# Optimization experiments

Measured on AMD Instinct MI355X. Metric: run time of the kernel, lower is better.

The kernel has to match this reference:

```python
import jax, jax.numpy as jnp
import numpy as np

B, S, D = 4, 2048, 1024


def setup_inputs() -> dict:
    key = jax.random.key(0)
    k1, k2, k3, k4, k5 = jax.random.split(key, 5)
    x = jax.random.normal(k1, (B, S, D), dtype=jnp.float32)
    mask = jax.random.randint(k2, (B, S), 0, 2).astype(jnp.bool_)
    # glorot-uniform-like init as keras add_weight default
    lim = float(np.sqrt(6.0 / (D + D)))
    q_w = jax.random.uniform(k3, (D, D), minval=-lim, maxval=lim, dtype=jnp.float32)
    k_w = jax.random.uniform(k4, (D, D), minval=-lim, maxval=lim, dtype=jnp.float32)
    v_w = jax.random.uniform(k5, (D, D), minval=-lim, maxval=lim, dtype=jnp.float32)
    return {"x": x, "mask": mask, "q_w": q_w, "k_w": k_w, "v_w": v_w}


def reference(x, mask, q_w, k_w, v_w):
    scale = 1.0 / jnp.sqrt(jnp.asarray(x.shape[-1], dtype=x.dtype))
    q = jnp.einsum('bsi,ij->bsj', x, q_w)
    k = jnp.einsum('bsi,ij->bsj', x, k_w)
    y = jnp.einsum('bsi,bzi->bsz', q, k) * scale  # [B,S,S] scores
    # additive mask applied along the query axis, exactly as the source
    m = (~mask).astype(x.dtype)[:, :, None]
    y = y + m * (-1e9)
    v = jnp.einsum('bsi,ij->bsj', x, v_w)
    p = jax.nn.softmax(y, axis=-1)
    return jnp.einsum('bsz,bzi->bsi', p, v)
```

## Files before the change

### kernel.cpp

```cpp
#include <hip/hip_runtime.h>
#include <hip/hip_bf16.h>

typedef __attribute__((ext_vector_type(8))) short short8;
typedef __attribute__((ext_vector_type(4))) float floatx4;

struct ushort4v { unsigned short x, y, z, w; };

static __device__ __forceinline__ unsigned short f2bf(float f) {
    __hip_bfloat16 h = __float2bfloat16(f);
    return *reinterpret_cast<unsigned short*>(&h);
}

static __device__ __forceinline__ float bf2f(unsigned short u) {
    unsigned int v = ((unsigned int)u) << 16;
    return *reinterpret_cast<float*>(&v);
}

#define ASYNC_COPY16(gsrc, ldst)                                                            \
    __builtin_amdgcn_global_load_lds((const __attribute__((address_space(1))) void*)(gsrc), \
                                     (__attribute__((address_space(3))) void*)(ldst), 16, 0, 0)

static __device__ __forceinline__ void block_barrier() {
    asm volatile("" ::: "memory");
    __builtin_amdgcn_s_barrier();
    asm volatile("" ::: "memory");
}

__global__ void mask_detect(const unsigned char* __restrict__ m, int* __restrict__ flag) {
    __shared__ int s_or;
    if (threadIdx.x == 0) s_or = 0;
    __syncthreads();
    int acc = 0;
    for (int i = threadIdx.x; i < 8192; i += 256)
        if (i & 3) acc |= m[i];
    atomicOr(&s_or, acc);
    __syncthreads();
    if (threadIdx.x == 0) *flag = (s_or != 0) ? 1 : 0;
}

__global__ void mask_expand(const void* __restrict__ m, const int* __restrict__ flag,
                            float* __restrict__ keep, int n) {
    int i = blockIdx.x * 256 + threadIdx.x;
    if (i >= n) return;
    bool on;
    if (*flag)
        on = ((const unsigned char*)m)[i] != 0;
    else
        on = ((const int*)m)[i] != 0;
    keep[i] = on ? 1.0f : 0.0f;
}

__global__ __launch_bounds__(256) void convert_f32_bf16(const float* __restrict__ in,
                                                        unsigned short* __restrict__ out, long n4) {
    long i = (long)blockIdx.x * 256 + threadIdx.x;
    if (i >= n4) return;
    float4 v = ((const float4*)in)[i];
    ushort4v o;
    o.x = f2bf(v.x); o.y = f2bf(v.y); o.z = f2bf(v.z); o.w = f2bf(v.w);
    ((ushort4v*)out)[i] = o;
}

__global__ void transpose_w_kernel(const float* __restrict__ w0, const float* __restrict__ w1,
                                   const float* __restrict__ w2, unsigned short* __restrict__ out) {
    __shared__ float t[32][33];
    const float* w = blockIdx.z == 0 ? w0 : (blockIdx.z == 1 ? w1 : w2);
    unsigned short* o = out + (long)blockIdx.z * 1024 * 1024;
    int c0 = blockIdx.x * 32, r0 = blockIdx.y * 32;
    for (int i = threadIdx.y; i < 32; i += 8)
        t[i][threadIdx.x] = w[(long)(r0 + i) * 1024 + c0 + threadIdx.x];
    __syncthreads();
    for (int i = threadIdx.y; i < 32; i += 8)
        o[(long)(c0 + i) * 1024 + r0 + threadIdx.x] = f2bf(t[threadIdx.x][i]);
}

__global__ void transpose_bf16(const unsigned short* __restrict__ in, unsigned short* __restrict__ out,
                               int rows, int cols, long sIn, long sOut) {
    __shared__ unsigned short t[32][34];
    const unsigned short* ib = in + (long)blockIdx.z * sIn;
    unsigned short* ob = out + (long)blockIdx.z * sOut;
    int c0 = blockIdx.x * 32, r0 = blockIdx.y * 32;
    for (int i = threadIdx.y; i < 32; i += 8)
        t[i][threadIdx.x] = ib[(long)(r0 + i) * cols + c0 + threadIdx.x];
    __syncthreads();
    for (int i = threadIdx.y; i < 32; i += 8)
        ob[(long)(c0 + i) * rows + r0 + threadIdx.x] = t[threadIdx.x][i];
}

template <int EPI, int BM>
static __device__ __forceinline__ void gemm8_body(const unsigned short* __restrict__ A,
                                                  const unsigned short* __restrict__ B,
                                                  void* __restrict__ Cv,
                                                  const float* __restrict__ aux,
                                                  int K, int lda, int ldb, int ldc,
                                                  long sA, long sB, long sC, long sAux,
                                                  float scale) {
    constexpr int M_REP = BM / 32;
    constexpr int LA    = BM * 128 / 8192;
    constexpr int LB    = 4;
    constexpr int TILE  = (BM + 256) * 128;
    __shared__ char sm[2 * TILE];

    const int tid = threadIdx.x;
    const int wid = tid >> 6, lane = tid & 63;
    const int wm  = wid >> 2, wn = wid & 3;
    const int fr  = lane & 15, fk = lane >> 4;
    const long m0 = (long)blockIdx.x * BM;
    const long n0 = (long)blockIdx.y * 256;
    const unsigned short* Ab = A + (long)blockIdx.z * sA + m0 * lda;
    const unsigned short* Bb = B + (long)blockIdx.z * sB + n0 * ldb;
    const int NT = K >> 6;

    floatx4 acc[M_REP][4] = {};

    auto stage = [&](int kt) {
        char* dA = sm + (kt & 1) * TILE;
        char* dB = dA + BM * 128;
        const int kb = kt << 6;
#pragma unroll
        for (int i = 0; i < LA; i++) {
            int lam = i * 8192 + tid * 16;
            int lg  = lam ^ (((lam >> 7) & 7) << 4);
            ASYNC_COPY16(Ab + (long)(lg >> 7) * lda + kb + ((lg & 127) >> 1), dA + lam);
        }
#pragma unroll
        for (int i = 0; i < LB; i++) {
            int lam = i * 8192 + tid * 16;
            int lg  = lam ^ (((lam >> 7) & 7) << 4);
            ASYNC_COPY16(Bb + (long)(lg >> 7) * ldb + kb + ((lg & 127) >> 1), dB + lam);
        }
    };

    stage(0);
    stage(1);

    for (int t = 0; t < NT; t++) {
        if (t + 1 < NT) {
            if constexpr (BM == 256) asm volatile("s_waitcnt vmcnt(8)" ::: "memory");
            else                     asm volatile("s_waitcnt vmcnt(6)" ::: "memory");
        } else {
            asm volatile("s_waitcnt vmcnt(0)" ::: "memory");
        }
        block_barrier();

        const char* bA = sm + (t & 1) * TILE;
        const char* bB = bA + BM * 128;
#pragma unroll
        for (int ks = 0; ks < 2; ks++) {
            short8 af[M_REP], bf[4];
#pragma unroll
            for (int mi = 0; mi < M_REP; mi++) {
                int row = wm * (BM / 2) + mi * 16 + fr;
                int c   = (ks * 64 + fk * 16) ^ ((row & 7) << 4);
                af[mi] = *(const short8*)(bA + row * 128 + c);
            }
#pragma unroll
            for (int ni = 0; ni < 4; ni++) {
                int row = wn * 64 + ni * 16 + fr;
                int c   = (ks * 64 + fk * 16) ^ ((row & 7) << 4);
                bf[ni] = *(const short8*)(bB + row * 128 + c);
            }
            __builtin_amdgcn_s_setprio(1);
#pragma unroll
            for (int mi = 0; mi < M_REP; mi++)
#pragma unroll
                for (int ni = 0; ni < 4; ni++)
                    acc[mi][ni] = __builtin_amdgcn_mfma_f32_16x16x32_bf16(af[mi], bf[ni], acc[mi][ni], 0, 0, 0);
            __builtin_amdgcn_s_setprio(0);
        }
        block_barrier();
        if (t + 2 < NT) stage(t + 2);
    }

    const int crow = (lane >> 4) * 4;
    const int ccol = lane & 15;
#pragma unroll
    for (int mi = 0; mi < M_REP; mi++) {
#pragma unroll
        for (int j = 0; j < 4; j++) {
            long r = m0 + wm * (BM / 2) + mi * 16 + crow + j;
            float rowf = 0.0f;
            if (EPI == 1) rowf = scale * aux[(long)blockIdx.z * sAux + r];
            if (EPI == 2) rowf = aux[(long)blockIdx.z * sAux + r];
#pragma unroll
            for (int ni = 0; ni < 4; ni++) {
                long c = n0 + wn * 64 + ni * 16 + ccol;
                float v = acc[mi][ni][j];
                if (EPI == 0) {
                    ((unsigned short*)Cv)[(long)blockIdx.z * sC + r * ldc + c] = f2bf(v);
                } else if (EPI == 1) {
                    ((unsigned short*)Cv)[(long)blockIdx.z * sC + r * ldc + c] = f2bf(__expf(v * rowf));
                } else {
                    ((float*)Cv)[(long)blockIdx.z * sC + r * ldc + c] = v * rowf;
                }
            }
        }
    }
}

__global__ __launch_bounds__(512, 2) void gemm8_qkv(const unsigned short* __restrict__ A,
                                                    const unsigned short* __restrict__ B,
                                                    void* __restrict__ Cv,
                                                    int K, int lda, int ldb, int ldc,
                                                    long sA, long sB, long sC) {
    gemm8_body<0, 128>(A, B, Cv, nullptr, K, lda, ldb, ldc, sA, sB, sC, 0L, 1.0f);
}

__global__ __launch_bounds__(512, 2) void gemm8_scores(const unsigned short* __restrict__ A,
                                                       const unsigned short* __restrict__ B,
                                                       void* __restrict__ Cv,
                                                       const float* __restrict__ keep,
                                                       int K, int lda, int ldb, int ldc,
                                                       long sA, long sB, long sC, long sAux,
                                                       float scale) {
    gemm8_body<1, 256>(A, B, Cv, keep, K, lda, ldb, ldc, sA, sB, sC, sAux, scale);
}

__global__ __launch_bounds__(512, 2) void gemm8_pv(const unsigned short* __restrict__ A,
                                                   const unsigned short* __restrict__ B,
                                                   void* __restrict__ Cv,
                                                   const float* __restrict__ invsum,
                                                   int K, int lda, int ldb, int ldc,
                                                   long sA, long sB, long sC, long sAux) {
    gemm8_body<2, 128>(A, B, Cv, invsum, K, lda, ldb, ldc, sA, sB, sC, sAux, 1.0f);
}

__global__ __launch_bounds__(256) void rowsum_inv(const unsigned short* __restrict__ P,
                                                  float* __restrict__ inv, long strideP) {
    const int tid = threadIdx.x;
    const long row = blockIdx.x;
    short8 v = ((const short8*)(P + row * strideP))[tid];
    float s = 0.0f;
#pragma unroll
    for (int i = 0; i < 8; i++) s += bf2f((unsigned short)v[i]);
#pragma unroll
    for (int i = 1; i < 64; i <<= 1) s += __shfl_xor(s, i);
    __shared__ float ss[4];
    if ((tid & 63) == 0) ss[tid >> 6] = s;
    __syncthreads();
    if (tid == 0) {
        float t = (ss[0] + ss[1]) + (ss[2] + ss[3]);
        inv[row] = 1.0f / t;
    }
}

extern "C" void kernel_launch(void* const* d_in, const int* in_sizes, int n_in,
                              void* d_out, int out_size, void* d_ws, size_t ws_size,
                              hipStream_t stream) {
    const float* x  = (const float*)d_in[0];
    const void*  mask = d_in[1];
    const float* qw = (const float*)d_in[2];
    const float* kw = (const float*)d_in[3];
    const float* vw = (const float*)d_in[4];
    float* out = (float*)d_out;

    constexpr int B = 4, S = 2048, D = 1024;
    constexpr long BS  = (long)B * S;
    constexpr long BSD = BS * D;

    char* w = (char*)d_ws;
    auto alloc = [&](size_t bytes) {
        char* p = w;
        w += (bytes + 255) & ~(size_t)255;
        return p;
    };
    int*            flag    = (int*)alloc(256);
    float*          keep    = (float*)alloc(BS * 4);
    float*          invsum  = (float*)alloc(BS * 4);
    unsigned short* xb      = (unsigned short*)alloc((size_t)BSD * 2);
    unsigned short* wT      = (unsigned short*)alloc((size_t)3 * D * D * 2);
    unsigned short* qkv     = (unsigned short*)alloc((size_t)3 * BSD * 2);
    unsigned short* Qb = qkv;
    unsigned short* Kb = qkv + BSD;
    unsigned short* Vb = qkv + 2 * BSD;
    unsigned short* Vt      = (unsigned short*)alloc((size_t)BSD * 2);

    size_t base_used = (size_t)(w - (char*)d_ws);
    size_t pB = (size_t)B * S * S * 2;
    bool batched = ws_size >= base_used + pB + 1024;

    unsigned short* P;
    if (batched) {
        P = (unsigned short*)alloc(pB);
    } else {
        P = (unsigned short*)alloc((size_t)S * S * 2);
    }

    const float scale = 0.03125f;

    mask_detect<<<1, 256, 0, stream>>>((const unsigned char*)mask, flag);
    mask_expand<<<(int)(BS / 256), 256, 0, stream>>>(mask, flag, keep, (int)BS);
    convert_f32_bf16<<<(int)(BSD / 1024), 256, 0, stream>>>(x, xb, BSD / 4);
    transpose_w_kernel<<<dim3(32, 32, 3), dim3(32, 8), 0, stream>>>(qw, kw, vw, wT);

    gemm8_qkv<<<dim3(64, 4, 3), 512, 0, stream>>>(xb, wT, qkv,
                                                  1024, 1024, 1024, 1024,
                                                  0L, (long)D * D, BSD);

    transpose_bf16<<<dim3(D / 32, S / 32, B), dim3(32, 8), 0, stream>>>(Vb, Vt, S, D,
                                                                        (long)S * D, (long)S * D);

    if (batched) {
        gemm8_scores<<<dim3(8, 8, B), 512, 0, stream>>>(Qb, Kb, P, keep,
                                                        1024, 1024, 1024, 2048,
                                                        (long)S * D, (long)S * D, (long)S * S, (long)S, scale);
        rowsum_inv<<<(int)BS, 256, 0, stream>>>(P, invsum, 2048);
        gemm8_pv<<<dim3(16, 4, B), 512, 0, stream>>>(P, Vt, out, invsum,
                                                     2048, 2048, 2048, 1024,
                                                     (long)S * S, (long)D * S, (long)S * D, (long)S);
    } else {
        for (int b = 0; b < B; b++) {
            gemm8_scores<<<dim3(8, 8, 1), 512, 0, stream>>>(Qb + (long)b * S * D, Kb + (long)b * S * D,
                                                            P, keep + (long)b * S,
                                                            1024, 1024, 1024, 2048,
                                                            0L, 0L, 0L, 0L, scale);
            rowsum_inv<<<S, 256, 0, stream>>>(P, invsum + (long)b * S, 2048);
            gemm8_pv<<<dim3(16, 4, 1), 512, 0, stream>>>(P, Vt + (long)b * D * S, out + (long)b * S * D,
                                                         invsum + (long)b * S,
                                                         2048, 2048, 2048, 1024,
                                                         0L, 0L, 0L, 0L);
        }
    }
}
```

Baseline: 187.7 us.

## Switch GEMMs to K=32 tiles with triple-buffered async LDS pipeline

The shared GEMM body moves from a double-buffered K=64 stage to a triple-buffered K=32 stage, with a new swizzle and matching vmcnt waits. The scores GEMM drops from BM=256 to BM=128 and its grid doubles, and launch bounds rise to 4 blocks per CU. The aim is to cut LDS per block so more blocks fit on each CU, and to keep more loads in flight to hide memory latency. In exchange there are twice as many barriers per unit of K, and the 4-block occupancy target may force register spills.

Measured after the change: 186.3 us. Within noise of the previous version (-0.8%).

```diff
diff --git a/kernel.cpp b/kernel.cpp
--- a/kernel.cpp
+++ b/kernel.cpp
@@ -86,7 +86,7 @@
         ob[(long)(c0 + i) * rows + r0 + threadIdx.x] = t[threadIdx.x][i];
 }
 
-template <int EPI, int BM>
+template <int EPI>
 static __device__ __forceinline__ void gemm8_body(const unsigned short* __restrict__ A,
                                                   const unsigned short* __restrict__ B,
                                                   void* __restrict__ Cv,
@@ -94,90 +94,84 @@
                                                   int K, int lda, int ldb, int ldc,
                                                   long sA, long sB, long sC, long sAux,
                                                   float scale) {
-    constexpr int M_REP = BM / 32;
-    constexpr int LA    = BM * 128 / 8192;
-    constexpr int LB    = 4;
-    constexpr int TILE  = (BM + 256) * 128;
-    __shared__ char sm[2 * TILE];
+    constexpr int TILE = (128 + 256) * 32 * 2;
+    __shared__ char sm[3 * TILE];
 
     const int tid = threadIdx.x;
     const int wid = tid >> 6, lane = tid & 63;
     const int wm  = wid >> 2, wn = wid & 3;
     const int fr  = lane & 15, fk = lane >> 4;
-    const long m0 = (long)blockIdx.x * BM;
+    const long m0 = (long)blockIdx.x * 128;
     const long n0 = (long)blockIdx.y * 256;
     const unsigned short* Ab = A + (long)blockIdx.z * sA + m0 * lda;
     const unsigned short* Bb = B + (long)blockIdx.z * sB + n0 * ldb;
-    const int NT = K >> 6;
-
-    floatx4 acc[M_REP][4] = {};
-
-    auto stage = [&](int kt) {
-        char* dA = sm + (kt & 1) * TILE;
-        char* dB = dA + BM * 128;
-        const int kb = kt << 6;
-#pragma unroll
-        for (int i = 0; i < LA; i++) {
+    const int NT = K >> 5;
+
+    floatx4 acc[4][4] = {};
+
+    auto stage = [&](int kt, int buf) {
+        char* dA = sm + buf * TILE;
+        char* dB = dA + 128 * 64;
+        const int kb = kt << 5;
+        {
+            int lam = tid * 16;
+            int lg  = lam ^ (((lam >> 7) & 3) << 4);
+            ASYNC_COPY16(Ab + (long)(lg >> 6) * lda + kb + ((lg & 63) >> 1), dA + lam);
+        }
+#pragma unroll
+        for (int i = 0; i < 2; i++) {
             int lam = i * 8192 + tid * 16;
-            int lg  = lam ^ (((lam >> 7) & 7) << 4);
-            ASYNC_COPY16(Ab + (long)(lg >> 7) * lda + kb + ((lg & 127) >> 1), dA + lam);
-        }
-#pragma unroll
-        for (int i = 0; i < LB; i++) {
-            int lam = i * 8192 + tid * 16;
-            int lg  = lam ^ (((lam >> 7) & 7) << 4);
-            ASYNC_COPY16(Bb + (long)(lg >> 7) * ldb + kb + ((lg & 127) >> 1), dB + lam);
+            int lg  = lam ^ (((lam >> 7) & 3) << 4);
+            ASYNC_COPY16(Bb + (long)(lg >> 6) * ldb + kb + ((lg & 63) >> 1), dB + lam);
         }
     };
 
-    stage(0);
-    stage(1);
-
+    stage(0, 0);
+    stage(1, 1);
+    stage(2, 2);
+
+    int cur = 0;
     for (int t = 0; t < NT; t++) {
-        if (t + 1 < NT) {
-            if constexpr (BM == 256) asm volatile("s_waitcnt vmcnt(8)" ::: "memory");
-            else                     asm volatile("s_waitcnt vmcnt(6)" ::: "memory");
-        } else {
-            asm volatile("s_waitcnt vmcnt(0)" ::: "memory");
-        }
+        const int nf = NT - 1 - t;
+        if (nf >= 2)      asm volatile("s_waitcnt vmcnt(6)" ::: "memory");
+        else if (nf == 1) asm volatile("s_waitcnt vmcnt(3)" ::: "memory");
+        else              asm volatile("s_waitcnt vmcnt(0)" ::: "memory");
         block_barrier();
 
-        const char* bA = sm + (t & 1) * TILE;
-        const char* bB = bA + BM * 128;
-#pragma unroll
-        for (int ks = 0; ks < 2; ks++) {
-            short8 af[M_REP], bf[4];
-#pragma unroll
-            for (int mi = 0; mi < M_REP; mi++) {
-                int row = wm * (BM / 2) + mi * 16 + fr;
-                int c   = (ks * 64 + fk * 16) ^ ((row & 7) << 4);
-                af[mi] = *(const short8*)(bA + row * 128 + c);
-            }
-#pragma unroll
-            for (int ni = 0; ni < 4; ni++) {
-                int row = wn * 64 + ni * 16 + fr;
-                int c   = (ks * 64 + fk * 16) ^ ((row & 7) << 4);
-                bf[ni] = *(const short8*)(bB + row * 128 + c);
-            }
-            __builtin_amdgcn_s_setprio(1);
-#pragma unroll
-            for (int mi = 0; mi < M_REP; mi++)
-#pragma unroll
-                for (int ni = 0; ni < 4; ni++)
-                    acc[mi][ni] = __builtin_amdgcn_mfma_f32_16x16x32_bf16(af[mi], bf[ni], acc[mi][ni], 0, 0, 0);
-            __builtin_amdgcn_s_setprio(0);
-        }
+        const char* bA = sm + cur * TILE;
+        const char* bB = bA + 128 * 64;
+        short8 af[4], bf[4];
+#pragma unroll
+        for (int mi = 0; mi < 4; mi++) {
+            int row = wm * 64 + mi * 16 + fr;
+            int c   = (fk * 16) ^ (((row >> 1) & 3) << 4);
+            af[mi] = *(const short8*)(bA + row * 64 + c);
+        }
+#pragma unroll
+        for (int ni = 0; ni < 4; ni++) {
+            int row = wn * 64 + ni * 16 + fr;
+            int c   = (fk * 16) ^ (((row >> 1) & 3) << 4);
+            bf[ni] = *(const short8*)(bB + row * 64 + c);
+        }
+        __builtin_amdgcn_s_setprio(1);
+#pragma unroll
+        for (int mi = 0; mi < 4; mi++)
+#pragma unroll
+            for (int ni = 0; ni < 4; ni++)
+                acc[mi][ni] = __builtin_amdgcn_mfma_f32_16x16x32_bf16(af[mi], bf[ni], acc[mi][ni], 0, 0, 0);
+        __builtin_amdgcn_s_setprio(0);
         block_barrier();
-        if (t + 2 < NT) stage(t + 2);
+        if (t + 3 < NT) stage(t + 3, cur);
+        cur = (cur == 2) ? 0 : cur + 1;
     }
 
     const int crow = (lane >> 4) * 4;
     const int ccol = lane & 15;
 #pragma unroll
-    for (int mi = 0; mi < M_REP; mi++) {
+    for (int mi = 0; mi < 4; mi++) {
 #pragma unroll
         for (int j = 0; j < 4; j++) {
-            long r = m0 + wm * (BM / 2) + mi * 16 + crow + j;
+            long r = m0 + wm * 64 + mi * 16 + crow + j;
             float rowf = 0.0f;
             if (EPI == 1) rowf = scale * aux[(long)blockIdx.z * sAux + r];
             if (EPI == 2) rowf = aux[(long)blockIdx.z * sAux + r];
@@ -197,31 +191,31 @@
     }
 }
 
-__global__ __launch_bounds__(512, 2) void gemm8_qkv(const unsigned short* __restrict__ A,
+__global__ __launch_bounds__(512, 4) void gemm8_qkv(const unsigned short* __restrict__ A,
                                                     const unsigned short* __restrict__ B,
                                                     void* __restrict__ Cv,
                                                     int K, int lda, int ldb, int ldc,
                                                     long sA, long sB, long sC) {
-    gemm8_body<0, 128>(A, B, Cv, nullptr, K, lda, ldb, ldc, sA, sB, sC, 0L, 1.0f);
-}
-
-__global__ __launch_bounds__(512, 2) void gemm8_scores(const unsigned short* __restrict__ A,
+    gemm8_body<0>(A, B, Cv, nullptr, K, lda, ldb, ldc, sA, sB, sC, 0L, 1.0f);
+}
+
+__global__ __launch_bounds__(512, 4) void gemm8_scores(const unsigned short* __restrict__ A,
                                                        const unsigned short* __restrict__ B,
                                                        void* __restrict__ Cv,
                                                        const float* __restrict__ keep,
                                                        int K, int lda, int ldb, int ldc,
                                                        long sA, long sB, long sC, long sAux,
                                                        float scale) {
-    gemm8_body<1, 256>(A, B, Cv, keep, K, lda, ldb, ldc, sA, sB, sC, sAux, scale);
-}
-
-__global__ __launch_bounds__(512, 2) void gemm8_pv(const unsigned short* __restrict__ A,
+    gemm8_body<1>(A, B, Cv, keep, K, lda, ldb, ldc, sA, sB, sC, sAux, scale);
+}
+
+__global__ __launch_bounds__(512, 4) void gemm8_pv(const unsigned short* __restrict__ A,
                                                    const unsigned short* __restrict__ B,
                                                    void* __restrict__ Cv,
                                                    const float* __restrict__ invsum,
                                                    int K, int lda, int ldb, int ldc,
                                                    long sA, long sB, long sC, long sAux) {
-    gemm8_body<2, 128>(A, B, Cv, invsum, K, lda, ldb, ldc, sA, sB, sC, sAux, 1.0f);
+    gemm8_body<2>(A, B, Cv, invsum, K, lda, ldb, ldc, sA, sB, sC, sAux, 1.0f);
 }
 
 __global__ __launch_bounds__(256) void rowsum_inv(const unsigned short* __restrict__ P,
@@ -300,19 +294,19 @@
                                                                         (long)S * D, (long)S * D);
 
     if (batched) {
-        gemm8_scores<<<dim3(8, 8, B), 512, 0, stream>>>(Qb, Kb, P, keep,
-                                                        1024, 1024, 1024, 2048,
-                                                        (long)S * D, (long)S * D, (long)S * S, (long)S, scale);
+        gemm8_scores<<<dim3(16, 8, B), 512, 0, stream>>>(Qb, Kb, P, keep,
+                                                         1024, 1024, 1024, 2048,
+                                                         (long)S * D, (long)S * D, (long)S * S, (long)S, scale);
         rowsum_inv<<<(int)BS, 256, 0, stream>>>(P, invsum, 2048);
         gemm8_pv<<<dim3(16, 4, B), 512, 0, stream>>>(P, Vt, out, invsum,
                                                      2048, 2048, 2048, 1024,
                                                      (long)S * S, (long)D * S, (long)S * D, (long)S);
     } else {
         for (int b = 0; b < B; b++) {
-            gemm8_scores<<<dim3(8, 8, 1), 512, 0, stream>>>(Qb + (long)b * S * D, Kb + (long)b * S * D,
-                                                            P, keep + (long)b * S,
-                                                            1024, 1024, 1024, 2048,
-                                                            0L, 0L, 0L, 0L, scale);
+            gemm8_scores<<<dim3(16, 8, 1), 512, 0, stream>>>(Qb + (long)b * S * D, Kb + (long)b * S * D,
+                                                             P, keep + (long)b * S,
+                                                             1024, 1024, 1024, 2048,
+                                                             0L, 0L, 0L, 0L, scale);
             rowsum_inv<<<S, 256, 0, stream>>>(P, invsum + (long)b * S, 2048);
             gemm8_pv<<<dim3(16, 4, 1), 512, 0, stream>>>(P, Vt + (long)b * D * S, out + (long)b * S * D,
                                                          invsum + (long)b * S,
```
